# Performance work log

Hardware: AMD Instinct MI355X
Metric: run time of the kernel (lower is better)

## Reference

```python
import jax, jax.numpy as jnp
import numpy as np

N = 40000      # nodes
E = 640000     # edges (avg degree 16)
IN_DIM = 128
OUT_DIM = 128
HEADS = 4
NEG_SLOPE = 0.01  # torch F.leaky_relu default


def lrelu(x):
    return jnp.where(x >= 0, x, NEG_SLOPE * x)


def gat_layer(h, fc_W, attn_W, edge_w, m_w, src, dst, pd):
    """One GATLayer: z = lrelu(fc(h)); per-edge score; segment softmax over dst; weighted sum.
    fc_W: [D_out, D_in], attn_W: [1, 2*D_out], edge_w/m_w: [1,1] scalars, pd: [E,1]."""
    n = h.shape[0]
    z = lrelu(h @ fc_W.T)                      # [N, D]
    d = z.shape[1]
    # attn_fc(cat(z_src, z_dst)) = z_src@a_l + z_dst@a_r  (no bias)
    a_src = z @ attn_W[0, :d]                  # [N]
    a_dst = z @ attn_W[0, d:]                  # [N]
    a = a_src[src] + a_dst[dst]                # [E]
    ev = pd[:, 0] * edge_w[0, 0]               # edge_fc (Linear(1,1), no bias)
    e = lrelu(a * ev)                          # [E]
    ne = e * m_w[0, 0]                         # m_fc (Linear(1,1), no bias)
    # segment softmax over destination node (DGL mailbox softmax)
    m = jax.ops.segment_max(ne, dst, num_segments=n)
    m = jnp.where(jnp.isfinite(m), m, 0.0)     # empty mailboxes -> 0
    ex = jnp.exp(ne - m[dst])                  # [E]
    s = jax.ops.segment_sum(ex, dst, num_segments=n)
    denom = jnp.where(s > 0, s, 1.0)
    alpha = ex / denom[dst]                    # [E]
    # h_i = sum_j alpha_ij * z_j  (scatter-add over dst)
    return jax.ops.segment_sum(alpha[:, None] * z[src], dst, num_segments=n)


def gru_cell(x, hprev, Wih, Whh, bih, bhh):
    """torch.nn.GRUCell math. Wih/Whh: [3H, H]; gate order: reset, update, new."""
    gi = x @ Wih.T + bih
    gh = hprev @ Whh.T + bhh
    ir, iz, in_ = jnp.split(gi, 3, axis=1)
    hr, hz, hn = jnp.split(gh, 3, axis=1)
    r = jax.nn.sigmoid(ir + hr)
    zg = jax.nn.sigmoid(iz + hz)
    ng = jnp.tanh(in_ + r * hn)
    return (1.0 - zg) * ng + zg * hprev


def setup_inputs() -> dict:
    key = jax.random.key(0)
    ks = jax.random.split(key, 16)
    sc = 0.05
    inp = {
        "h": jax.random.normal(ks[0], (N, IN_DIM), jnp.float32),
        "pd": jax.random.uniform(ks[1], (E, 1), jnp.float32),
        "src": jax.random.randint(ks[2], (E,), 0, N, jnp.int32),
        "dst": jax.random.randint(ks[3], (E,), 0, N, jnp.int32),
        # per-head GATLayer params, stacked on leading head axis
        "fc_W": jax.random.normal(ks[4], (HEADS, OUT_DIM, IN_DIM), jnp.float32) * sc,
        "attn_W": jax.random.normal(ks[5], (HEADS, 1, 2 * OUT_DIM), jnp.float32) * sc,
        "edge_w": jax.random.normal(ks[6], (HEADS, 1, 1), jnp.float32) * sc + 1.0,
        "m_w": jax.random.normal(ks[7], (HEADS, 1, 1), jnp.float32) * sc + 1.0,
        # output GATLayer (in = HEADS*OUT_DIM)
        "out_fc_W": jax.random.normal(ks[8], (OUT_DIM, HEADS * OUT_DIM), jnp.float32) * sc,
        "out_attn_W": jax.random.normal(ks[9], (1, 2 * OUT_DIM), jnp.float32) * sc,
        "out_edge_w": jax.random.normal(ks[10], (1, 1), jnp.float32) * sc + 1.0,
        "out_m_w": jax.random.normal(ks[11], (1, 1), jnp.float32) * sc + 1.0,
        # GRUCell(OUT_DIM, OUT_DIM)
        "gru_Wih": jax.random.normal(ks[12], (3 * OUT_DIM, OUT_DIM), jnp.float32) * sc,
        "gru_Whh": jax.random.normal(ks[13], (3 * OUT_DIM, OUT_DIM), jnp.float32) * sc,
        "gru_bih": jax.random.normal(ks[14], (3 * OUT_DIM,), jnp.float32) * sc,
        "gru_bhh": jax.random.normal(ks[15], (3 * OUT_DIM,), jnp.float32) * sc,
    }
    return inp


def reference(h, pd, fc_W, attn_W, edge_w, m_w,
              out_fc_W, out_attn_W, out_edge_w, out_m_w,
              gru_Wih, gru_Whh, gru_bih, gru_bhh,
              src, dst):
    gru_in = h  # in_dim == out_dim -> no transform
    heads = [gat_layer(h, fc_W[i], attn_W[i], edge_w[i], m_w[i], src, dst, pd)
             for i in range(HEADS)]
    x = lrelu(jnp.concatenate(heads, axis=1))          # [N, HEADS*OUT_DIM]
    x = lrelu(gat_layer(x, out_fc_W, out_attn_W, out_edge_w, out_m_w, src, dst, pd))
    x = lrelu(gru_cell(x, gru_in, gru_Wih, gru_Whh, gru_bih, gru_bhh))
    return x
```

## Files before the change

### kernel.cpp

```cpp
#include <hip/hip_runtime.h>
#include <math.h>

#define NEG_SLOPE 0.01f

__device__ __forceinline__ float lrelu_f(float x) { return x >= 0.f ? x : NEG_SLOPE * x; }

typedef __attribute__((ext_vector_type(8))) short short8v;
typedef __attribute__((ext_vector_type(4))) short short4v;
typedef __attribute__((ext_vector_type(4))) float f32x4;

__device__ __forceinline__ unsigned short f2bf(float f) {
  unsigned u = __float_as_uint(f);
  u += 0x7FFF + ((u >> 16) & 1);
  return (unsigned short)(u >> 16);
}
__device__ __forceinline__ float bf2f(unsigned short s) {
  return __uint_as_float((unsigned)s << 16);
}

template<int TN, bool LRELU, bool BIAS>
__global__ __launch_bounds__(256)
void gemm_bf16x3(const float* __restrict__ A, const float* __restrict__ B,
                 const float* __restrict__ bias, float* __restrict__ C,
                 int M, int Nn, int K) {
  constexpr int MI = (TN == 128) ? 4 : 2;
  constexpr int NI = 4;
  __shared__ short AsH[128 * 64], AsL[128 * 64];
  __shared__ short BsH[TN * 64],  BsL[TN * 64];
  const int tid = threadIdx.x;
  const int lane = tid & 63, w = tid >> 6;
  const int tx = tid & 15, ty = tid >> 4;
  const int bm = blockIdx.y << 7, bn = blockIdx.x * TN;
  const int m0 = (TN == 128) ? (w >> 1) * 64 : w * 32;
  const int n0 = (TN == 128) ? (w & 1) * 64 : 0;
  const int sbase = (tx >> 3) * 32 + (tx & 3) * 8 + ((tx >> 2) & 1) * 4;
  const int g = lane >> 4;
  const int key = (lane & 7) << 3;
  const int arow = lane & 15;

  f32x4 acc[MI][NI];
#pragma unroll
  for (int i = 0; i < MI; ++i)
#pragma unroll
    for (int j = 0; j < NI; ++j) acc[i][j] = (f32x4){0.f, 0.f, 0.f, 0.f};

  for (int k0 = 0; k0 < K; k0 += 64) {
#pragma unroll
    for (int i = 0; i < 8; ++i) {
      const int r = ty + (i << 4);
      int ar = bm + r; ar = ar < M ? ar : M - 1;
      const float4 va = *(const float4*)(A + (size_t)ar * K + k0 + (tx << 2));
      short4v h, l;
      h[0] = (short)f2bf(va.x); l[0] = (short)f2bf(va.x - bf2f(h[0]));
      h[1] = (short)f2bf(va.y); l[1] = (short)f2bf(va.y - bf2f(h[1]));
      h[2] = (short)f2bf(va.z); l[2] = (short)f2bf(va.z - bf2f(h[2]));
      h[3] = (short)f2bf(va.w); l[3] = (short)f2bf(va.w - bf2f(h[3]));
      const int idx = r * 64 + (sbase ^ ((r & 7) << 3));
      *(short4v*)&AsH[idx] = h;
      *(short4v*)&AsL[idx] = l;
    }
#pragma unroll
    for (int i = 0; i < TN / 16; ++i) {
      const int r = ty + (i << 4);
      const float4 vb = *(const float4*)(B + (size_t)(bn + r) * K + k0 + (tx << 2));
      short4v h, l;
      h[0] = (short)f2bf(vb.x); l[0] = (short)f2bf(vb.x - bf2f(h[0]));
      h[1] = (short)f2bf(vb.y); l[1] = (short)f2bf(vb.y - bf2f(h[1]));
      h[2] = (short)f2bf(vb.z); l[2] = (short)f2bf(vb.z - bf2f(h[2]));
      h[3] = (short)f2bf(vb.w); l[3] = (short)f2bf(vb.w - bf2f(h[3]));
      const int idx = r * 64 + (sbase ^ ((r & 7) << 3));
      *(short4v*)&BsH[idx] = h;
      *(short4v*)&BsL[idx] = l;
    }
    __syncthreads();
#pragma unroll
    for (int kh = 0; kh < 2; ++kh) {
      const int sb = kh * 32 + g * 8;
      short8v aH[MI], aL[MI], bH[NI], bL[NI];
#pragma unroll
      for (int mi = 0; mi < MI; ++mi) {
        const int base = (m0 + arow + mi * 16) * 64 + (sb ^ key);
        aH[mi] = *(const short8v*)&AsH[base];
        aL[mi] = *(const short8v*)&AsL[base];
      }
#pragma unroll
      for (int ni = 0; ni < NI; ++ni) {
        const int base = (n0 + arow + ni * 16) * 64 + (sb ^ key);
        bH[ni] = *(const short8v*)&BsH[base];
        bL[ni] = *(const short8v*)&BsL[base];
      }
#pragma unroll
      for (int mi = 0; mi < MI; ++mi)
#pragma unroll
        for (int ni = 0; ni < NI; ++ni) {
          acc[mi][ni] = __builtin_amdgcn_mfma_f32_16x16x32_bf16(aH[mi], bH[ni], acc[mi][ni], 0, 0, 0);
          acc[mi][ni] = __builtin_amdgcn_mfma_f32_16x16x32_bf16(aH[mi], bL[ni], acc[mi][ni], 0, 0, 0);
          acc[mi][ni] = __builtin_amdgcn_mfma_f32_16x16x32_bf16(aL[mi], bH[ni], acc[mi][ni], 0, 0, 0);
        }
    }
    __syncthreads();
  }

  const int rg = (lane >> 4) << 2;
#pragma unroll
  for (int ni = 0; ni < NI; ++ni) {
    const int col = bn + n0 + ni * 16 + (lane & 15);
    const float bc = BIAS ? bias[col] : 0.f;
#pragma unroll
    for (int mi = 0; mi < MI; ++mi) {
#pragma unroll
      for (int r4 = 0; r4 < 4; ++r4) {
        const int row = bm + m0 + mi * 16 + rg + r4;
        if (row < M) {
          float v = acc[mi][ni][r4] + bc;
          if (LRELU) v = lrelu_f(v);
          C[(size_t)row * Nn + col] = v;
        }
      }
    }
  }
}

__global__ __launch_bounds__(256)
void attn_heads_k(const float* __restrict__ z, const float* __restrict__ attnW,
                  float* __restrict__ asrc, float* __restrict__ adst, int N) {
  const int wid = (int)((blockIdx.x * (unsigned)blockDim.x + threadIdx.x) >> 6);
  const int lane = threadIdx.x & 63;
  if (wid >= N) return;
  const int h = lane >> 4;
  const int dd = (lane & 15) << 3;
  const float* zp = z + (size_t)wid * 512 + h * 128 + dd;
  const float* aw = attnW + h * 256 + dd;
  const float4 z0 = *(const float4*)zp;
  const float4 z1 = *(const float4*)(zp + 4);
  const float4 w0 = *(const float4*)aw;
  const float4 w1 = *(const float4*)(aw + 4);
  const float4 w2 = *(const float4*)(aw + 128);
  const float4 w3 = *(const float4*)(aw + 132);
  float ps = z0.x * w0.x + z0.y * w0.y + z0.z * w0.z + z0.w * w0.w
           + z1.x * w1.x + z1.y * w1.y + z1.z * w1.z + z1.w * w1.w;
  float pq = z0.x * w2.x + z0.y * w2.y + z0.z * w2.z + z0.w * w2.w
           + z1.x * w3.x + z1.y * w3.y + z1.z * w3.z + z1.w * w3.w;
#pragma unroll
  for (int off = 8; off; off >>= 1) {
    ps += __shfl_xor(ps, off);
    pq += __shfl_xor(pq, off);
  }
  if ((lane & 15) == 0) {
    asrc[(size_t)h * N + wid] = ps;
    adst[(size_t)h * N + wid] = pq;
  }
}

__global__ __launch_bounds__(256)
void attn_out_k(const float* __restrict__ z2, const float* __restrict__ attnW,
                float* __restrict__ asrc, float* __restrict__ adst, int N) {
  const int wid = (int)((blockIdx.x * (unsigned)blockDim.x + threadIdx.x) >> 6);
  const int lane = threadIdx.x & 63;
  if (wid >= N) return;
  const float* zp = z2 + (size_t)wid * 128;
  const float za = zp[lane], zb = zp[lane + 64];
  float ps = za * attnW[lane] + zb * attnW[lane + 64];
  float pq = za * attnW[128 + lane] + zb * attnW[192 + lane];
#pragma unroll
  for (int off = 32; off; off >>= 1) {
    ps += __shfl_xor(ps, off);
    pq += __shfl_xor(pq, off);
  }
  if (lane == 0) {
    asrc[wid] = ps;
    adst[wid] = pq;
  }
}

__global__ void hist_k(const int* __restrict__ dst, int* __restrict__ deg, int E) {
  const int i = blockIdx.x * 256 + threadIdx.x;
  if (i < E) atomicAdd(&deg[dst[i]], 1);
}

__global__ __launch_bounds__(1024)
void scan_k(const int* __restrict__ deg, int* __restrict__ ptr, int n) {
  __shared__ int wsum[16];
  __shared__ int carry_s;
  const int tid = threadIdx.x;
  const int lane = tid & 63, wv = tid >> 6;
  if (tid == 0) carry_s = 0;
  __syncthreads();
  for (int base = 0; base < n; base += 1024) {
    const int i = base + tid;
    int s = (i < n) ? deg[i] : 0;
#pragma unroll
    for (int off = 1; off < 64; off <<= 1) {
      const int t = __shfl_up(s, off);
      if (lane >= off) s += t;
    }
    if (lane == 63) wsum[wv] = s;
    __syncthreads();
    if (wv == 0 && lane < 16) {
      int ws = wsum[lane];
#pragma unroll
      for (int off = 1; off < 16; off <<= 1) {
        const int t = __shfl_up(ws, off);
        if (lane >= off) ws += t;
      }
      wsum[lane] = ws;
    }
    __syncthreads();
    const int wprefix = (wv == 0) ? 0 : wsum[wv - 1];
    const int carry = carry_s;
    if (i < n) ptr[i + 1] = carry + wprefix + s;
    __syncthreads();
    if (tid == 1023) carry_s = carry + wsum[15];
    __syncthreads();
  }
  if (tid == 0) ptr[0] = 0;
}

__global__ void scatter_k(const int* __restrict__ dst, const int* __restrict__ src,
                          const float* __restrict__ pd, const int* __restrict__ ptr,
                          int* __restrict__ cursor,
                          int* __restrict__ src_s, float* __restrict__ pd_s, int E) {
  const int i = blockIdx.x * 256 + threadIdx.x;
  if (i < E) {
    const int d = dst[i];
    const int p = ptr[d] + atomicAdd(&cursor[d], 1);
    src_s[p] = src[i];
    pd_s[p] = pd[i];
  }
}

__global__ __launch_bounds__(256)
void gat_aggregate(const float* __restrict__ z, int ldz, int zHS,
                   const float* __restrict__ asrc, const float* __restrict__ adst, int aHS,
                   const float* __restrict__ pd_s,
                   const float* __restrict__ ewp, const float* __restrict__ mwp, int sHS,
                   const int* __restrict__ src_s, const int* __restrict__ csr_ptr,
                   float* __restrict__ outp, int ldo, int oHS, int N) {
  __shared__ float pair[4][128][2];
  const int hd = blockIdx.y;
  z += (size_t)hd * zHS;
  asrc += (size_t)hd * aHS;
  adst += (size_t)hd * aHS;
  outp += (size_t)hd * oHS;
  const int wib = threadIdx.x >> 6;
  const int wid = blockIdx.x * 4 + wib;
  const int lane = threadIdx.x & 63;
  if (wid >= N) return;
  const int rs = csr_ptr[wid], re = csr_ptr[wid + 1];
  const int deg = re - rs;
  const int l32 = lane & 31;
  const int half = lane >> 5;
  float* op = outp + (size_t)wid * ldo;
  if (deg == 0) {
    if (half == 0) *(float4*)(op + (l32 << 2)) = make_float4(0.f, 0.f, 0.f, 0.f);
    return;
  }
  const float ew = ewp[hd * sHS];
  const float mw = mwp[hd * sHS];
  const float adn = adst[wid];

  float ne0 = -INFINITY, ne1 = -INFINITY;
  int s0 = 0, s1 = 0;
  {
    int j = rs + lane;
    if (j < re) {
      s0 = src_s[j];
      ne0 = mw * lrelu_f((asrc[s0] + adn) * (pd_s[j] * ew));
    }
    j += 64;
    if (j < re) {
      s1 = src_s[j];
      ne1 = mw * lrelu_f((asrc[s1] + adn) * (pd_s[j] * ew));
    }
  }
  float m = fmaxf(ne0, ne1);
  for (int j = rs + 128 + lane; j < re; j += 64) {
    const int s = src_s[j];
    m = fmaxf(m, mw * lrelu_f((asrc[s] + adn) * (pd_s[j] * ew)));
  }
#pragma unroll
  for (int off = 32; off; off >>= 1) m = fmaxf(m, __shfl_xor(m, off));

  const float ex0 = expf(ne0 - m);
  const float ex1 = expf(ne1 - m);
  float ss = ex0 + ex1;
  for (int j = rs + 128 + lane; j < re; j += 64) {
    const int s = src_s[j];
    ss += expf(mw * lrelu_f((asrc[s] + adn) * (pd_s[j] * ew)) - m);
  }
#pragma unroll
  for (int off = 32; off; off >>= 1) ss += __shfl_xor(ss, off);

  pair[wib][lane][0] = ex0;
  pair[wib][lane][1] = __int_as_float(s0);
  pair[wib][lane + 64][0] = ex1;
  pair[wib][lane + 64][1] = __int_as_float(s1);

  float a0 = 0.f, a1 = 0.f, a2 = 0.f, a3 = 0.f;
  const int zoff = l32 << 2;
  for (int q0 = 0; q0 < deg; q0 += 8) {
#pragma unroll
    for (int u = 0; u < 4; ++u) {
      const int q = q0 + (u << 1) + half;
      float exv; int sv;
      if (q < deg) {
        if (q < 128) {
          const float2 p = *(const float2*)&pair[wib][q][0];
          exv = p.x; sv = __float_as_int(p.y);
        } else {
          sv = src_s[rs + q];
          exv = expf(mw * lrelu_f((asrc[sv] + adn) * (pd_s[rs + q] * ew)) - m);
        }
      } else {
        exv = 0.f; sv = 0;
      }
      const float4 zv = *(const float4*)(z + (size_t)sv * ldz + zoff);
      a0 = fmaf(exv, zv.x, a0);
      a1 = fmaf(exv, zv.y, a1);
      a2 = fmaf(exv, zv.z, a2);
      a3 = fmaf(exv, zv.w, a3);
    }
  }
  a0 += __shfl_xor(a0, 32);
  a1 += __shfl_xor(a1, 32);
  a2 += __shfl_xor(a2, 32);
  a3 += __shfl_xor(a3, 32);
  if (half == 0) {
    const float rd = 1.f / ((ss > 0.f) ? ss : 1.f);
    *(float4*)(op + zoff) = make_float4(lrelu_f(a0 * rd), lrelu_f(a1 * rd),
                                        lrelu_f(a2 * rd), lrelu_f(a3 * rd));
  }
}

__global__ __launch_bounds__(256)
void gru_gate_k(const float* __restrict__ gi, const float* __restrict__ gh,
                const float* __restrict__ h, float* __restrict__ out, int total) {
  const int i = blockIdx.x * 256 + threadIdx.x;
  if (i >= total) return;
  const int n = i >> 7, d = i & 127;
  const float* gin = gi + (size_t)n * 384;
  const float* ghn = gh + (size_t)n * 384;
  const float r = 1.f / (1.f + expf(-(gin[d] + ghn[d])));
  const float zg = 1.f / (1.f + expf(-(gin[128 + d] + ghn[128 + d])));
  const float ng = tanhf(gin[256 + d] + r * ghn[256 + d]);
  const float v = (1.f - zg) * ng + zg * h[i];
  out[i] = lrelu_f(v);
}

extern "C" void kernel_launch(void* const* d_in, const int* in_sizes, int n_in,
                              void* d_out, int out_size, void* d_ws, size_t ws_size,
                              hipStream_t stream) {
  const int N = in_sizes[0] / 128;
  const int E = in_sizes[1];

  const float* h     = (const float*)d_in[0];
  const float* pd    = (const float*)d_in[1];
  const int*   src   = (const int*)d_in[2];
  const int*   dst   = (const int*)d_in[3];
  const float* fcW   = (const float*)d_in[4];
  const float* attnW = (const float*)d_in[5];
  const float* edgew = (const float*)d_in[6];
  const float* mw    = (const float*)d_in[7];
  const float* ofcW  = (const float*)d_in[8];
  const float* oattn = (const float*)d_in[9];
  const float* oew   = (const float*)d_in[10];
  const float* omw   = (const float*)d_in[11];
  const float* Wih   = (const float*)d_in[12];
  const float* Whh   = (const float*)d_in[13];
  const float* bih   = (const float*)d_in[14];
  const float* bhh   = (const float*)d_in[15];
  float* out = (float*)d_out;

  char* w = (char*)d_ws;
  size_t off = 0;
  auto alloc = [&](size_t bytes) -> char* {
    char* p = w + off;
    off += (bytes + 255) & ~(size_t)255;
    return p;
  };
  float* z     = (float*)alloc((size_t)N * 512 * 4);
  float* x     = (float*)alloc((size_t)N * 512 * 4);
  float* z2    = (float*)alloc((size_t)N * 128 * 4);
  float* asrc  = (float*)alloc((size_t)4 * N * 4);
  float* adst  = (float*)alloc((size_t)4 * N * 4);
  float* a2s   = (float*)alloc((size_t)N * 4);
  float* a2d   = (float*)alloc((size_t)N * 4);
  int* deg     = (int*)alloc((size_t)N * 4);
  int* ptr     = (int*)alloc((size_t)(N + 1) * 4);
  int* cursor  = (int*)alloc((size_t)N * 4);
  int* src_s   = (int*)alloc((size_t)E * 4);
  float* pd_s  = (float*)alloc((size_t)E * 4);
  float* gi = z;
  float* gh = x;
  float* x2 = out;
  (void)ws_size; (void)n_in; (void)out_size;

  const int nodeBlocks = (N + 3) / 4;
  const int eBlocks = (E + 255) / 256;
  const int mBlocks = (N + 127) / 128;

  gemm_bf16x3<128, true, false><<<dim3(512 / 128, mBlocks), 256, 0, stream>>>(h, fcW, nullptr, z, N, 512, 128);

  attn_heads_k<<<nodeBlocks, 256, 0, stream>>>(z, attnW, asrc, adst, N);

  hipMemsetAsync(deg, 0, (size_t)N * 4, stream);
  hipMemsetAsync(cursor, 0, (size_t)N * 4, stream);
  hist_k<<<eBlocks, 256, 0, stream>>>(dst, deg, E);
  scan_k<<<1, 1024, 0, stream>>>(deg, ptr, N);
  scatter_k<<<eBlocks, 256, 0, stream>>>(dst, src, pd, ptr, cursor, src_s, pd_s, E);

  gat_aggregate<<<dim3(nodeBlocks, 4), 256, 0, stream>>>(
      z, 512, 128, asrc, adst, N, pd_s, edgew, mw, 1, src_s, ptr, x, 512, 128, N);

  gemm_bf16x3<64, true, false><<<dim3(128 / 64, mBlocks), 256, 0, stream>>>(x, ofcW, nullptr, z2, N, 128, 512);

  attn_out_k<<<nodeBlocks, 256, 0, stream>>>(z2, oattn, a2s, a2d, N);

  gat_aggregate<<<dim3(nodeBlocks, 1), 256, 0, stream>>>(
      z2, 128, 0, a2s, a2d, 0, pd_s, oew, omw, 0, src_s, ptr, x2, 128, 0, N);

  gemm_bf16x3<64, false, true><<<dim3(384 / 64, mBlocks), 256, 0, stream>>>(x2, Wih, bih, gi, N, 384, 128);
  gemm_bf16x3<64, false, true><<<dim3(384 / 64, mBlocks), 256, 0, stream>>>(h, Whh, bhh, gh, N, 384, 128);

  gru_gate_k<<<(N * 128 + 255) / 256, 256, 0, stream>>>(gi, gh, h, out, N * 128);
}
```

Before: 658.2 us.

## Pre-split GEMM operands to bf16 hi/lo, gather fp16 features, fuse head aggregation

After: 612.4 us. 7.0% less time.

```diff
diff --git a/kernel.cpp b/kernel.cpp
--- a/kernel.cpp
+++ b/kernel.cpp
@@ -8,6 +8,8 @@
 typedef __attribute__((ext_vector_type(8))) short short8v;
 typedef __attribute__((ext_vector_type(4))) short short4v;
 typedef __attribute__((ext_vector_type(4))) float f32x4;
+typedef __attribute__((ext_vector_type(8))) _Float16 half8v;
+typedef __attribute__((ext_vector_type(4))) _Float16 half4v;
 
 __device__ __forceinline__ unsigned short f2bf(float f) {
   unsigned u = __float_as_uint(f);
@@ -18,11 +20,28 @@
   return __uint_as_float((unsigned)s << 16);
 }
 
-template<int TN, bool LRELU, bool BIAS>
-__global__ __launch_bounds__(256)
-void gemm_bf16x3(const float* __restrict__ A, const float* __restrict__ B,
+__global__ __launch_bounds__(256)
+void split_bf16_k(const float* __restrict__ in, short* __restrict__ H,
+                  short* __restrict__ L, int n4) {
+  const int stride = gridDim.x * 256;
+  for (int i = blockIdx.x * 256 + threadIdx.x; i < n4; i += stride) {
+    const float4 v = ((const float4*)in)[i];
+    short4v h, l;
+    h[0] = (short)f2bf(v.x); l[0] = (short)f2bf(v.x - bf2f(h[0]));
+    h[1] = (short)f2bf(v.y); l[1] = (short)f2bf(v.y - bf2f(h[1]));
+    h[2] = (short)f2bf(v.z); l[2] = (short)f2bf(v.z - bf2f(h[2]));
+    h[3] = (short)f2bf(v.w); l[3] = (short)f2bf(v.w - bf2f(h[3]));
+    ((short4v*)H)[i] = h;
+    ((short4v*)L)[i] = l;
+  }
+}
+
+template<int TN, bool LRELU, bool BIAS, bool HOUT>
+__global__ __launch_bounds__(256)
+void gemm_bf16x3(const short* __restrict__ AH, const short* __restrict__ AL,
+                 const short* __restrict__ BH, const short* __restrict__ BL,
                  const float* __restrict__ bias, float* __restrict__ C,
-                 int M, int Nn, int K) {
+                 _Float16* __restrict__ Ch, int M, int Nn, int K) {
   constexpr int MI = (TN == 128) ? 4 : 2;
   constexpr int NI = 4;
   __shared__ short AsH[128 * 64], AsL[128 * 64];
@@ -49,12 +68,9 @@
     for (int i = 0; i < 8; ++i) {
       const int r = ty + (i << 4);
       int ar = bm + r; ar = ar < M ? ar : M - 1;
-      const float4 va = *(const float4*)(A + (size_t)ar * K + k0 + (tx << 2));
-      short4v h, l;
-      h[0] = (short)f2bf(va.x); l[0] = (short)f2bf(va.x - bf2f(h[0]));
-      h[1] = (short)f2bf(va.y); l[1] = (short)f2bf(va.y - bf2f(h[1]));
-      h[2] = (short)f2bf(va.z); l[2] = (short)f2bf(va.z - bf2f(h[2]));
-      h[3] = (short)f2bf(va.w); l[3] = (short)f2bf(va.w - bf2f(h[3]));
+      const size_t go = (size_t)ar * K + k0 + (tx << 2);
+      const short4v h = *(const short4v*)(AH + go);
+      const short4v l = *(const short4v*)(AL + go);
       const int idx = r * 64 + (sbase ^ ((r & 7) << 3));
       *(short4v*)&AsH[idx] = h;
       *(short4v*)&AsL[idx] = l;
@@ -62,12 +78,9 @@
 #pragma unroll
     for (int i = 0; i < TN / 16; ++i) {
       const int r = ty + (i << 4);
-      const float4 vb = *(const float4*)(B + (size_t)(bn + r) * K + k0 + (tx << 2));
-      short4v h, l;
-      h[0] = (short)f2bf(vb.x); l[0] = (short)f2bf(vb.x - bf2f(h[0]));
-      h[1] = (short)f2bf(vb.y); l[1] = (short)f2bf(vb.y - bf2f(h[1]));
-      h[2] = (short)f2bf(vb.z); l[2] = (short)f2bf(vb.z - bf2f(h[2]));
-      h[3] = (short)f2bf(vb.w); l[3] = (short)f2bf(vb.w - bf2f(h[3]));
+      const size_t go = (size_t)(bn + r) * K + k0 + (tx << 2);
+      const short4v h = *(const short4v*)(BH + go);
+      const short4v l = *(const short4v*)(BL + go);
       const int idx = r * 64 + (sbase ^ ((r & 7) << 3));
       *(short4v*)&BsH[idx] = h;
       *(short4v*)&BsL[idx] = l;
@@ -115,6 +128,7 @@
           float v = acc[mi][ni][r4] + bc;
           if (LRELU) v = lrelu_f(v);
           C[(size_t)row * Nn + col] = v;
+          if (HOUT) Ch[(size_t)row * Nn + col] = (_Float16)v;
         }
       }
     }
@@ -230,18 +244,120 @@
 }
 
 __global__ __launch_bounds__(256)
-void gat_aggregate(const float* __restrict__ z, int ldz, int zHS,
-                   const float* __restrict__ asrc, const float* __restrict__ adst, int aHS,
-                   const float* __restrict__ pd_s,
-                   const float* __restrict__ ewp, const float* __restrict__ mwp, int sHS,
-                   const int* __restrict__ src_s, const int* __restrict__ csr_ptr,
-                   float* __restrict__ outp, int ldo, int oHS, int N) {
+void gat_heads_fused(const _Float16* __restrict__ zh,
+                     const float* __restrict__ asrc, const float* __restrict__ adst,
+                     const float* __restrict__ pd_s,
+                     const float* __restrict__ ewp, const float* __restrict__ mwp,
+                     const int* __restrict__ src_s, const int* __restrict__ csr_ptr,
+                     float* __restrict__ outp, int N) {
+  __shared__ float pair[4][128][5];
+  const int wib = threadIdx.x >> 6;
+  const int wid = blockIdx.x * 4 + wib;
+  const int lane = threadIdx.x & 63;
+  if (wid >= N) return;
+  const int rs = csr_ptr[wid], re = csr_ptr[wid + 1];
+  const int deg = re - rs;
+  const int hh = lane >> 4;
+  const int c = lane << 3;
+  float* op = outp + (size_t)wid * 512 + c;
+  if (deg == 0) {
+    *(float4*)op = make_float4(0.f, 0.f, 0.f, 0.f);
+    *(float4*)(op + 4) = make_float4(0.f, 0.f, 0.f, 0.f);
+    return;
+  }
+  float ew[4], mwv[4], adn[4];
+#pragma unroll
+  for (int h = 0; h < 4; ++h) {
+    ew[h] = ewp[h]; mwv[h] = mwp[h];
+    adn[h] = adst[(size_t)h * N + wid];
+  }
+  const int j0 = rs + lane, j1 = j0 + 64;
+  const bool v0 = j0 < re, v1 = j1 < re;
+  const int s0 = v0 ? src_s[j0] : 0;
+  const float p0 = v0 ? pd_s[j0] : 0.f;
+  const int s1 = v1 ? src_s[j1] : 0;
+  const float p1 = v1 ? pd_s[j1] : 0.f;
+  float ne0[4], ne1[4], m[4];
+#pragma unroll
+  for (int h = 0; h < 4; ++h) {
+    const float a0 = asrc[(size_t)h * N + s0];
+    const float a1 = asrc[(size_t)h * N + s1];
+    ne0[h] = v0 ? mwv[h] * lrelu_f((a0 + adn[h]) * (p0 * ew[h])) : -INFINITY;
+    ne1[h] = v1 ? mwv[h] * lrelu_f((a1 + adn[h]) * (p1 * ew[h])) : -INFINITY;
+    m[h] = fmaxf(ne0[h], ne1[h]);
+  }
+  for (int j = rs + 128 + lane; j < re; j += 64) {
+    const int s = src_s[j];
+    const float p = pd_s[j];
+#pragma unroll
+    for (int h = 0; h < 4; ++h)
+      m[h] = fmaxf(m[h], mwv[h] * lrelu_f((asrc[(size_t)h * N + s] + adn[h]) * (p * ew[h])));
+  }
+#pragma unroll
+  for (int h = 0; h < 4; ++h)
+#pragma unroll
+    for (int off = 32; off; off >>= 1) m[h] = fmaxf(m[h], __shfl_xor(m[h], off));
+
+  float ss[4];
+#pragma unroll
+  for (int h = 0; h < 4; ++h) {
+    const float e0 = expf(ne0[h] - m[h]);
+    const float e1 = expf(ne1[h] - m[h]);
+    pair[wib][lane][h] = e0;
+    pair[wib][lane + 64][h] = e1;
+    ss[h] = e0 + e1;
+  }
+  pair[wib][lane][4] = __int_as_float(s0);
+  pair[wib][lane + 64][4] = __int_as_float(s1);
+  for (int j = rs + 128 + lane; j < re; j += 64) {
+    const int s = src_s[j];
+    const float p = pd_s[j];
+#pragma unroll
+    for (int h = 0; h < 4; ++h)
+      ss[h] += expf(mwv[h] * lrelu_f((asrc[(size_t)h * N + s] + adn[h]) * (p * ew[h])) - m[h]);
+  }
+#pragma unroll
+  for (int h = 0; h < 4; ++h)
+#pragma unroll
+    for (int off = 32; off; off >>= 1) ss[h] += __shfl_xor(ss[h], off);
+
+  float a[8] = {0.f, 0.f, 0.f, 0.f, 0.f, 0.f, 0.f, 0.f};
+  for (int q0 = 0; q0 < deg; q0 += 2) {
+#pragma unroll
+    for (int u = 0; u < 2; ++u) {
+      const int q = q0 + u;
+      float exv; int sv;
+      if (q < deg) {
+        if (q < 128) {
+          exv = pair[wib][q][hh];
+          sv = __float_as_int(pair[wib][q][4]);
+        } else {
+          sv = src_s[rs + q];
+          exv = expf(mwv[hh] * lrelu_f((asrc[(size_t)hh * N + sv] + adn[hh]) * (pd_s[rs + q] * ew[hh])) - m[hh]);
+        }
+      } else {
+        exv = 0.f; sv = 0;
+      }
+      const half8v zv = *(const half8v*)(zh + (size_t)sv * 512 + c);
+#pragma unroll
+      for (int t = 0; t < 8; ++t) a[t] = fmaf(exv, (float)zv[t], a[t]);
+    }
+  }
+  const float rd = 1.f / ((ss[hh] > 0.f) ? ss[hh] : 1.f);
+  *(float4*)op = make_float4(lrelu_f(a[0] * rd), lrelu_f(a[1] * rd),
+                             lrelu_f(a[2] * rd), lrelu_f(a[3] * rd));
+  *(float4*)(op + 4) = make_float4(lrelu_f(a[4] * rd), lrelu_f(a[5] * rd),
+                                   lrelu_f(a[6] * rd), lrelu_f(a[7] * rd));
+}
+
+__global__ __launch_bounds__(256)
+void gat_out_aggregate(const _Float16* __restrict__ zh,
+                       const float* __restrict__ asrc, const float* __restrict__ adst,
+                       const float* __restrict__ pd_s,
+                       const float* __restrict__ ewp, const float* __restrict__ mwp,
+                       const int* __restrict__ src_s, const int* __restrict__ csr_ptr,
+                       float* __restrict__ outp, int N) {
   __shared__ float pair[4][128][2];
-  const int hd = blockIdx.y;
-  z += (size_t)hd * zHS;
-  asrc += (size_t)hd * aHS;
-  adst += (size_t)hd * aHS;
-  outp += (size_t)hd * oHS;
   const int wib = threadIdx.x >> 6;
   const int wid = blockIdx.x * 4 + wib;
   const int lane = threadIdx.x & 63;
@@ -250,13 +366,13 @@
   const int deg = re - rs;
   const int l32 = lane & 31;
   const int half = lane >> 5;
-  float* op = outp + (size_t)wid * ldo;
+  float* op = outp + (size_t)wid * 128;
   if (deg == 0) {
     if (half == 0) *(float4*)(op + (l32 << 2)) = make_float4(0.f, 0.f, 0.f, 0.f);
     return;
   }
-  const float ew = ewp[hd * sHS];
-  const float mw = mwp[hd * sHS];
+  const float ew = ewp[0];
+  const float mw = mwp[0];
   const float adn = adst[wid];
 
   float ne0 = -INFINITY, ne1 = -INFINITY;
@@ -298,9 +414,9 @@
 
   float a0 = 0.f, a1 = 0.f, a2 = 0.f, a3 = 0.f;
   const int zoff = l32 << 2;
-  for (int q0 = 0; q0 < deg; q0 += 8) {
-#pragma unroll
-    for (int u = 0; u < 4; ++u) {
+  for (int q0 = 0; q0 < deg; q0 += 4) {
+#pragma unroll
+    for (int u = 0; u < 2; ++u) {
       const int q = q0 + (u << 1) + half;
       float exv; int sv;
       if (q < deg) {
@@ -314,11 +430,11 @@
       } else {
         exv = 0.f; sv = 0;
       }
-      const float4 zv = *(const float4*)(z + (size_t)sv * ldz + zoff);
-      a0 = fmaf(exv, zv.x, a0);
-      a1 = fmaf(exv, zv.y, a1);
-      a2 = fmaf(exv, zv.z, a2);
-      a3 = fmaf(exv, zv.w, a3);
+      const half4v zv = *(const half4v*)(zh + (size_t)sv * 128 + zoff);
+      a0 = fmaf(exv, (float)zv[0], a0);
+      a1 = fmaf(exv, (float)zv[1], a1);
+      a2 = fmaf(exv, (float)zv[2], a2);
+      a3 = fmaf(exv, (float)zv[3], a3);
     }
   }
   a0 += __shfl_xor(a0, 32);
@@ -378,9 +494,21 @@
     off += (bytes + 255) & ~(size_t)255;
     return p;
   };
-  float* z     = (float*)alloc((size_t)N * 512 * 4);
-  float* x     = (float*)alloc((size_t)N * 512 * 4);
+  char* regA = alloc((size_t)N * 512 * 4);
+  float* z   = (float*)regA;
+  short* xH  = (short*)regA;
+  short* xL  = (short*)(regA + (size_t)N * 512 * 2);
+  float* gh  = (float*)regA;
+  char* regB = alloc((size_t)N * 512 * 4);
+  float* x   = (float*)regB;
+  short* x2H = (short*)regB;
+  short* x2L = (short*)(regB + (size_t)N * 128 * 2);
+  float* gi  = (float*)(regB + (size_t)N * 128 * 4);
+  _Float16* zh  = (_Float16*)alloc((size_t)N * 512 * 2);
+  _Float16* z2h = (_Float16*)alloc((size_t)N * 128 * 2);
   float* z2    = (float*)alloc((size_t)N * 128 * 4);
+  short* hH    = (short*)alloc((size_t)N * 128 * 2);
+  short* hL    = (short*)alloc((size_t)N * 128 * 2);
   float* asrc  = (float*)alloc((size_t)4 * N * 4);
   float* adst  = (float*)alloc((size_t)4 * N * 4);
   float* a2s   = (float*)alloc((size_t)N * 4);
@@ -390,8 +518,14 @@
   int* cursor  = (int*)alloc((size_t)N * 4);
   int* src_s   = (int*)alloc((size_t)E * 4);
   float* pd_s  = (float*)alloc((size_t)E * 4);
-  float* gi = z;
-  float* gh = x;
+  short* fcWH  = (short*)alloc((size_t)512 * 128 * 2);
+  short* fcWL  = (short*)alloc((size_t)512 * 128 * 2);
+  short* ofcWH = (short*)alloc((size_t)128 * 512 * 2);
+  short* ofcWL = (short*)alloc((size_t)128 * 512 * 2);
+  short* WihH  = (short*)alloc((size_t)384 * 128 * 2);
+  short* WihL  = (short*)alloc((size_t)384 * 128 * 2);
+  short* WhhH  = (short*)alloc((size_t)384 * 128 * 2);
+  short* WhhL  = (short*)alloc((size_t)384 * 128 * 2);
   float* x2 = out;
   (void)ws_size; (void)n_in; (void)out_size;
 
@@ -399,7 +533,14 @@
   const int eBlocks = (E + 255) / 256;
   const int mBlocks = (N + 127) / 128;
 
-  gemm_bf16x3<128, true, false><<<dim3(512 / 128, mBlocks), 256, 0, stream>>>(h, fcW, nullptr, z, N, 512, 128);
+  split_bf16_k<<<512, 256, 0, stream>>>(h, hH, hL, N * 128 / 4);
+  split_bf16_k<<<64, 256, 0, stream>>>(fcW, fcWH, fcWL, 512 * 128 / 4);
+  split_bf16_k<<<64, 256, 0, stream>>>(ofcW, ofcWH, ofcWL, 128 * 512 / 4);
+  split_bf16_k<<<48, 256, 0, stream>>>(Wih, WihH, WihL, 384 * 128 / 4);
+  split_bf16_k<<<48, 256, 0, stream>>>(Whh, WhhH, WhhL, 384 * 128 / 4);
+
+  gemm_bf16x3<128, true, false, true><<<dim3(512 / 128, mBlocks), 256, 0, stream>>>(
+      hH, hL, fcWH, fcWL, nullptr, z, zh, N, 512, 128);
 
   attn_heads_k<<<nodeBlocks, 256, 0, stream>>>(z, attnW, asrc, adst, N);
 
@@ -409,18 +550,25 @@
   scan_k<<<1, 1024, 0, stream>>>(deg, ptr, N);
   scatter_k<<<eBlocks, 256, 0, stream>>>(dst, src, pd, ptr, cursor, src_s, pd_s, E);
 
-  gat_aggregate<<<dim3(nodeBlocks, 4), 256, 0, stream>>>(
-      z, 512, 128, asrc, adst, N, pd_s, edgew, mw, 1, src_s, ptr, x, 512, 128, N);
-
-  gemm_bf16x3<64, true, false><<<dim3(128 / 64, mBlocks), 256, 0, stream>>>(x, ofcW, nullptr, z2, N, 128, 512);
+  gat_heads_fused<<<nodeBlocks, 256, 0, stream>>>(
+      zh, asrc, adst, pd_s, edgew, mw, src_s, ptr, x, N);
+
+  split_bf16_k<<<2048, 256, 0, stream>>>(x, xH, xL, N * 512 / 4);
+
+  gemm_bf16x3<64, true, false, true><<<dim3(128 / 64, mBlocks), 256, 0, stream>>>(
+      xH, xL, ofcWH, ofcWL, nullptr, z2, z2h, N, 128, 512);
 
   attn_out_k<<<nodeBlocks, 256, 0, stream>>>(z2, oattn, a2s, a2d, N);
 
-  gat_aggregate<<<dim3(nodeBlocks, 1), 256, 0, stream>>>(
-      z2, 128, 0, a2s, a2d, 0, pd_s, oew, omw, 0, src_s, ptr, x2, 128, 0, N);
-
-  gemm_bf16x3<64, false, true><<<dim3(384 / 64, mBlocks), 256, 0, stream>>>(x2, Wih, bih, gi, N, 384, 128);
-  gemm_bf16x3<64, false, true><<<dim3(384 / 64, mBlocks), 256, 0, stream>>>(h, Whh, bhh, gh, N, 384, 128);
+  gat_out_aggregate<<<nodeBlocks, 256, 0, stream>>>(
+      z2h, a2s, a2d, pd_s, oew, omw, src_s, ptr, x2, N);
+
+  split_bf16_k<<<512, 256, 0, stream>>>(x2, x2H, x2L, N * 128 / 4);
+
+  gemm_bf16x3<64, false, true, false><<<dim3(384 / 64, mBlocks), 256, 0, stream>>>(
+      x2H, x2L, WihH, WihL, bih, gi, nullptr, N, 384, 128);
+  gemm_bf16x3<64, false, true, false><<<dim3(384 / 64, mBlocks), 256, 0, stream>>>(
+      hH, hL, WhhH, WhhL, bhh, gh, nullptr, N, 384, 128);
 
   gru_gate_k<<<(N * 128 + 255) / 256, 256, 0, stream>>>(gi, gh, h, out, N * 128);
 }
```
